# Performance work log

Hardware: AMD Instinct MI355X
Metric: run time of the kernel (lower is better)

Reference implementation:

```python
import jax, jax.numpy as jnp
import numpy as np

H = 4           # LSTM hidden size
T = 200         # seq len (T * H == 800, required by the reshape)
FEAT = 800      # flattened feature size into the linear
OUT = 28        # linear output dim


def run_lstm_layer(x, Wih, Whh, bih, bhh):
    """Single LSTM layer, PyTorch gate order (i, f, g, o). x: [B, T, I] -> [B, T, H]."""
    B = x.shape[0]
    xT = jnp.swapaxes(x, 0, 1)  # [T, B, I]
    h0 = jnp.zeros((B, H), x.dtype)
    c0 = jnp.zeros((B, H), x.dtype)
    b = bih + bhh  # [4H]

    def step(carry, xt):
        h, c = carry
        gates = xt @ Wih.T + h @ Whh.T + b  # [B, 4H]
        i, f, g, o = jnp.split(gates, 4, axis=-1)
        i = jax.nn.sigmoid(i)
        f = jax.nn.sigmoid(f)
        g = jnp.tanh(g)
        o = jax.nn.sigmoid(o)
        c = f * c + i * g
        h = o * jnp.tanh(c)
        return (h, c), h

    _, hs = jax.lax.scan(step, (h0, c0), xT)  # hs: [T, B, H]
    return jnp.swapaxes(hs, 0, 1)  # [B, T, H]


def setup_inputs() -> dict:
    key = jax.random.key(0)
    ks = jax.random.split(key, 12)
    B, I = 32768, 4
    s_lstm = 1.0 / np.sqrt(H)     # torch LSTM init bound
    s_lin = 1.0 / np.sqrt(FEAT)   # torch Linear init bound

    def u(k, shape, s):
        return jax.random.uniform(k, shape, jnp.float32, -s, s)

    return {
        "x": jax.random.normal(ks[0], (B, T, I), jnp.float32),
        "Wih0": u(ks[1], (4 * H, I), s_lstm),
        "Whh0": u(ks[2], (4 * H, H), s_lstm),
        "bih0": u(ks[3], (4 * H,), s_lstm),
        "bhh0": u(ks[4], (4 * H,), s_lstm),
        "Wih1": u(ks[5], (4 * H, H), s_lstm),
        "Whh1": u(ks[6], (4 * H, H), s_lstm),
        "bih1": u(ks[7], (4 * H,), s_lstm),
        "bhh1": u(ks[8], (4 * H,), s_lstm),
        "Wout": u(ks[9], (OUT, FEAT), s_lin),
        "bout": u(ks[10], (OUT,), s_lin),
    }


def reference(x, Wih0, Whh0, bih0, bhh0, Wih1, Whh1, bih1, bhh1, Wout, bout):
    h1 = run_lstm_layer(x, Wih0, Whh0, bih0, bhh0)   # [B, T, H]
    h2 = run_lstm_layer(h1, Wih1, Whh1, bih1, bhh1)  # [B, T, H]
    feat = h2.reshape(-1, FEAT)                      # [B, 800] since T*H == 800
    return feat @ Wout.T + bout                      # [B, 28]
```

## Files before the change

kernel.cpp:

```cpp
#include <hip/hip_runtime.h>

#define T_STEPS 200
#define OUTD 28

typedef float f2 __attribute__((ext_vector_type(2)));

template<int SRC>
__device__ __forceinline__ float qb(float v) {
    return __int_as_float(__builtin_amdgcn_update_dpp(
        0, __float_as_int(v), SRC * 0x55, 0xF, 0xF, true));
}

#define PIN2(v) asm volatile("" : "+v"(v))

__global__ void transpose_wout(const float* __restrict__ Wout, float* __restrict__ Wt) {
    int idx = blockIdx.x * 256 + threadIdx.x;
    if (idx < T_STEPS * OUTD * 4) {
        int t = idx / (OUTD * 4);
        int r = idx - t * (OUTD * 4);
        int j = r >> 2, c = r & 3;
        Wt[idx] = Wout[j * 800 + 4 * t + c];
    }
}

__device__ __forceinline__ void layer_step2(const f2 (&wia)[4], const f2 (&wib)[4],
                                            const f2 (&wha)[4], const f2 (&whb)[4],
                                            const f2 (&bb)[4],
                                            f2 ina0, f2 inb0, f2 ina1, f2 inb1,
                                            f2& ha0, f2& hb0, f2& ha1, f2& hb1,
                                            float& c0, float& c1)
{
    float g0[4], g1[4];
#pragma unroll
    for (int gi = 0; gi < 4; ++gi) {
        f2 s0 = bb[gi];
        f2 s1 = bb[gi];
        s0 += wia[gi] * ina0;  s1 += wia[gi] * ina1;
        s0 += wib[gi] * inb0;  s1 += wib[gi] * inb1;
        s0 += wha[gi] * ha0;   s1 += wha[gi] * ha1;
        s0 += whb[gi] * hb0;   s1 += whb[gi] * hb1;
        g0[gi] = s0.x + s0.y;  g1[gi] = s1.x + s1.y;
    }
    float Ei0 = __builtin_amdgcn_exp2f(g0[0]), Ei1 = __builtin_amdgcn_exp2f(g1[0]);
    float Ef0 = __builtin_amdgcn_exp2f(g0[1]), Ef1 = __builtin_amdgcn_exp2f(g1[1]);
    float Eg0 = __builtin_amdgcn_exp2f(g0[2]), Eg1 = __builtin_amdgcn_exp2f(g1[2]);
    float Eo0 = __builtin_amdgcn_exp2f(g0[3]), Eo1 = __builtin_amdgcn_exp2f(g1[3]);
    float Ai0 = 1.0f + Ei0,  Ai1 = 1.0f + Ei1;
    float Af0 = 1.0f + Ef0,  Af1 = 1.0f + Ef1;
    float Ag0 = 1.0f + Eg0,  Ag1 = 1.0f + Eg1;
    float Ao0 = 1.0f + Eo0,  Ao1 = 1.0f + Eo1;
    float P0 = Ai0 * Ag0,    P1 = Ai1 * Ag1;
    float n0 = c0 * P0 + (Eg0 - 1.0f) * Af0;
    float n1 = c1 * P1 + (Eg1 - 1.0f) * Af1;
    float r0 = __builtin_amdgcn_rcpf(P0 * Af0);
    float r1 = __builtin_amdgcn_rcpf(P1 * Af1);
    c0 = n0 * r0;
    c1 = n1 * r1;
    float cc0 = __builtin_amdgcn_fmed3f(c0, -16.0f, 16.0f);
    float cc1 = __builtin_amdgcn_fmed3f(c1, -16.0f, 16.0f);
    float Ec0 = __builtin_amdgcn_exp2f(2.8853900817779268f * cc0);
    float Ec1 = __builtin_amdgcn_exp2f(2.8853900817779268f * cc1);
    float q0 = __builtin_amdgcn_rcpf(Ao0 * (1.0f + Ec0));
    float q1 = __builtin_amdgcn_rcpf(Ao1 * (1.0f + Ec1));
    float ho0 = (Ec0 - 1.0f) * q0;
    float ho1 = (Ec1 - 1.0f) * q1;
    ha0 = f2{qb<0>(ho0), qb<1>(ho0)};
    ha1 = f2{qb<0>(ho1), qb<1>(ho1)};
    hb0 = f2{qb<2>(ho0), qb<3>(ho0)};
    hb1 = f2{qb<2>(ho1), qb<3>(ho1)};
}

template<bool PREF>
__device__ __forceinline__ void full_step(
    const f2 (&wi0a)[4], const f2 (&wi0b)[4], const f2 (&wh0a)[4], const f2 (&wh0b)[4],
    const f2 (&wi1a)[4], const f2 (&wi1b)[4], const f2 (&wh1a)[4], const f2 (&wh1b)[4],
    const f2 (&b0)[4], const f2 (&b1)[4],
    f2& h1a0, f2& h1b0, f2& h2a0, f2& h2b0, float& c10, float& c20,
    f2& h1a1, f2& h1b1, f2& h2a1, f2& h2b1, float& c11, float& c21,
    f2 (&acc0)[7], f2 (&acc1)[7],
    float4& xs0, float4& xs1,
    const char* xp, unsigned xo0, unsigned xo1, int tpf,
    const char* wtp, unsigned w_off)
{
    float4 wo[7];
#pragma unroll
    for (int jj = 0; jj < 7; ++jj)
        wo[jj] = *(const float4*)(wtp + w_off + jj * 16);

    f2 xa0 = f2{xs0.x, xs0.y}, xb0 = f2{xs0.z, xs0.w};
    f2 xa1 = f2{xs1.x, xs1.y}, xb1 = f2{xs1.z, xs1.w};

    layer_step2(wi0a, wi0b, wh0a, wh0b, b0,
                xa0, xb0, xa1, xb1,
                h1a0, h1b0, h1a1, h1b1, c10, c11);

    if (PREF) {
        xs0 = *(const float4*)(xp + xo0 + (size_t)tpf * 16);
        xs1 = *(const float4*)(xp + xo1 + (size_t)tpf * 16);
    }

    layer_step2(wi1a, wi1b, wh1a, wh1b, b1,
                h1a0, h1b0, h1a1, h1b1,
                h2a0, h2b0, h2a1, h2b1, c20, c21);

#pragma unroll
    for (int jj = 0; jj < 7; ++jj) {
        f2 wa = f2{wo[jj].x, wo[jj].y};
        f2 wb = f2{wo[jj].z, wo[jj].w};
        acc0[jj] += wa * h2a0; acc0[jj] += wb * h2b0;
        acc1[jj] += wa * h2a1; acc1[jj] += wb * h2b1;
    }
}

__global__ __launch_bounds__(256)
__attribute__((amdgpu_waves_per_eu(1, 1)))
void lstm2_fused(const float* __restrict__ x,
                 const float* __restrict__ Wih0, const float* __restrict__ Whh0,
                 const float* __restrict__ bih0, const float* __restrict__ bhh0,
                 const float* __restrict__ Wih1, const float* __restrict__ Whh1,
                 const float* __restrict__ bih1, const float* __restrict__ bhh1,
                 const float* __restrict__ Wt,   const float* __restrict__ bout,
                 float* __restrict__ out, int batch)
{
    const int tid = blockIdx.x * 256 + threadIdx.x;
    const int quad = tid >> 2;
    const int k = tid & 3;
    const int e0 = quad * 2, e1 = e0 + 1;
    if (e1 >= batch) return;

    f2 wi0a[4], wi0b[4], wh0a[4], wh0b[4];
    f2 wi1a[4], wi1b[4], wh1a[4], wh1b[4];
    f2 b0[4], b1[4];
#pragma unroll
    for (int gi = 0; gi < 4; ++gi) {
        const int row = gi * 4 + k;
        const float sc = (gi == 2) ? 2.8853900817779268f : -1.4426950408889634f;
        float4 a = ((const float4*)Wih0)[row];
        float4 c = ((const float4*)Whh0)[row];
        float4 d = ((const float4*)Wih1)[row];
        float4 e = ((const float4*)Whh1)[row];
        wi0a[gi] = f2{a.x * sc, a.y * sc}; wi0b[gi] = f2{a.z * sc, a.w * sc};
        wh0a[gi] = f2{c.x * sc, c.y * sc}; wh0b[gi] = f2{c.z * sc, c.w * sc};
        wi1a[gi] = f2{d.x * sc, d.y * sc}; wi1b[gi] = f2{d.z * sc, d.w * sc};
        wh1a[gi] = f2{e.x * sc, e.y * sc}; wh1b[gi] = f2{e.z * sc, e.w * sc};
        b0[gi] = f2{(bih0[row] + bhh0[row]) * sc, 0.0f};
        b1[gi] = f2{(bih1[row] + bhh1[row]) * sc, 0.0f};
    }
#pragma unroll
    for (int gi = 0; gi < 4; ++gi) {
        PIN2(wi0a[gi]); PIN2(wi0b[gi]); PIN2(wh0a[gi]); PIN2(wh0b[gi]);
        PIN2(wi1a[gi]); PIN2(wi1b[gi]); PIN2(wh1a[gi]); PIN2(wh1b[gi]);
        PIN2(b0[gi]);   PIN2(b1[gi]);
    }

    f2 acc0[7], acc1[7];
#pragma unroll
    for (int jj = 0; jj < 7; ++jj) {
        float bj = bout[k * 7 + jj];
        acc0[jj] = f2{bj, 0.0f};
        acc1[jj] = f2{bj, 0.0f};
    }

    f2 h1a0 = f2{0,0}, h1b0 = f2{0,0}, h2a0 = f2{0,0}, h2b0 = f2{0,0};
    f2 h1a1 = f2{0,0}, h1b1 = f2{0,0}, h2a1 = f2{0,0}, h2b1 = f2{0,0};
    float c10 = 0.0f, c20 = 0.0f, c11 = 0.0f, c21 = 0.0f;

    const char* xp  = (const char*)x;
    const unsigned xo0 = (unsigned)e0 * 3200u;
    const unsigned xo1 = (unsigned)e1 * 3200u;
    const char* wtp = (const char*)Wt;
    const unsigned w_off = (unsigned)k * 112u;

    float4 xv0 = *(const float4*)(xp + xo0);
    float4 xv1 = *(const float4*)(xp + xo1);
    float4 xn0 = *(const float4*)(xp + xo0 + 16);
    float4 xn1 = *(const float4*)(xp + xo1 + 16);

    for (int t = 0; t < T_STEPS - 2; t += 2) {
        full_step<true>(wi0a, wi0b, wh0a, wh0b, wi1a, wi1b, wh1a, wh1b, b0, b1,
                        h1a0, h1b0, h2a0, h2b0, c10, c20,
                        h1a1, h1b1, h2a1, h2b1, c11, c21,
                        acc0, acc1, xv0, xv1, xp, xo0, xo1, t + 2, wtp, w_off);
        wtp += OUTD * 16;
        full_step<true>(wi0a, wi0b, wh0a, wh0b, wi1a, wi1b, wh1a, wh1b, b0, b1,
                        h1a0, h1b0, h2a0, h2b0, c10, c20,
                        h1a1, h1b1, h2a1, h2b1, c11, c21,
                        acc0, acc1, xn0, xn1, xp, xo0, xo1, t + 3, wtp, w_off);
        wtp += OUTD * 16;
    }
    full_step<false>(wi0a, wi0b, wh0a, wh0b, wi1a, wi1b, wh1a, wh1b, b0, b1,
                     h1a0, h1b0, h2a0, h2b0, c10, c20,
                     h1a1, h1b1, h2a1, h2b1, c11, c21,
                     acc0, acc1, xv0, xv1, xp, xo0, xo1, 0, wtp, w_off);
    wtp += OUTD * 16;
    full_step<false>(wi0a, wi0b, wh0a, wh0b, wi1a, wi1b, wh1a, wh1b, b0, b1,
                     h1a0, h1b0, h2a0, h2b0, c10, c20,
                     h1a1, h1b1, h2a1, h2b1, c11, c21,
                     acc0, acc1, xn0, xn1, xp, xo0, xo1, 0, wtp, w_off);

    float* op0 = out + (size_t)e0 * OUTD + k * 7;
    float* op1 = out + (size_t)e1 * OUTD + k * 7;
#pragma unroll
    for (int jj = 0; jj < 7; ++jj) {
        op0[jj] = acc0[jj].x + acc0[jj].y;
        op1[jj] = acc1[jj].x + acc1[jj].y;
    }
}

extern "C" void kernel_launch(void* const* d_in, const int* in_sizes, int n_in,
                              void* d_out, int out_size, void* d_ws, size_t ws_size,
                              hipStream_t stream) {
    const float* x    = (const float*)d_in[0];
    const float* Wih0 = (const float*)d_in[1];
    const float* Whh0 = (const float*)d_in[2];
    const float* bih0 = (const float*)d_in[3];
    const float* bhh0 = (const float*)d_in[4];
    const float* Wih1 = (const float*)d_in[5];
    const float* Whh1 = (const float*)d_in[6];
    const float* bih1 = (const float*)d_in[7];
    const float* bhh1 = (const float*)d_in[8];
    const float* Wout = (const float*)d_in[9];
    const float* bout = (const float*)d_in[10];
    float* out = (float*)d_out;
    float* Wt  = (float*)d_ws;

    transpose_wout<<<(T_STEPS * OUTD * 4 + 255) / 256, 256, 0, stream>>>(Wout, Wt);

    const int batch = in_sizes[0] / (T_STEPS * 4);
    const int threads = (batch / 2) * 4;
    const int grid = threads / 256;
    lstm2_fused<<<grid, 256, 0, stream>>>(
        x, Wih0, Whh0, bih0, bhh0, Wih1, Whh1, bih1, bhh1, Wt, bout, out, batch);
}
```

Baseline: 234.9 us.

## Split LSTM layers across producer/consumer waves with LDS double-buffered pipeline

Each block now has 512 threads. Four waves compute layer 1 and four waves compute layer 2 one timestep behind, exchanging hidden states through double-buffered shared memory with a barrier per step. The output linear accumulation is split between the two wave groups, which lowers per-thread register pressure and gives more concurrent waves. The cost is a __syncthreads per timestep and extra LDS traffic, and batch must be divisible by 128.

```diff
diff --git a/kernel.cpp b/kernel.cpp
--- a/kernel.cpp
+++ b/kernel.cpp
@@ -23,12 +23,13 @@
     }
 }
 
-__device__ __forceinline__ void layer_step2(const f2 (&wia)[4], const f2 (&wib)[4],
-                                            const f2 (&wha)[4], const f2 (&whb)[4],
-                                            const f2 (&bb)[4],
-                                            f2 ina0, f2 inb0, f2 ina1, f2 inb1,
-                                            f2& ha0, f2& hb0, f2& ha1, f2& hb1,
-                                            float& c0, float& c1)
+__device__ __forceinline__ void layer_pair(const f2 (&wia)[4], const f2 (&wib)[4],
+                                           const f2 (&wha)[4], const f2 (&whb)[4],
+                                           const f2 (&bb)[4],
+                                           f2 ina0, f2 inb0, f2 ina1, f2 inb1,
+                                           f2& ha0, f2& hb0, f2& ha1, f2& hb1,
+                                           float& c0, float& c1,
+                                           float& o0, float& o1)
 {
     float g0[4], g1[4];
 #pragma unroll
@@ -56,64 +57,29 @@
     float r1 = __builtin_amdgcn_rcpf(P1 * Af1);
     c0 = n0 * r0;
     c1 = n1 * r1;
-    float cc0 = __builtin_amdgcn_fmed3f(c0, -16.0f, 16.0f);
-    float cc1 = __builtin_amdgcn_fmed3f(c1, -16.0f, 16.0f);
-    float Ec0 = __builtin_amdgcn_exp2f(2.8853900817779268f * cc0);
-    float Ec1 = __builtin_amdgcn_exp2f(2.8853900817779268f * cc1);
+    float cl0 = __builtin_amdgcn_fmed3f(c0, -16.0f, 16.0f);
+    float cl1 = __builtin_amdgcn_fmed3f(c1, -16.0f, 16.0f);
+    float Ec0 = __builtin_amdgcn_exp2f(2.8853900817779268f * cl0);
+    float Ec1 = __builtin_amdgcn_exp2f(2.8853900817779268f * cl1);
     float q0 = __builtin_amdgcn_rcpf(Ao0 * (1.0f + Ec0));
     float q1 = __builtin_amdgcn_rcpf(Ao1 * (1.0f + Ec1));
     float ho0 = (Ec0 - 1.0f) * q0;
     float ho1 = (Ec1 - 1.0f) * q1;
+    o0 = ho0;
+    o1 = ho1;
     ha0 = f2{qb<0>(ho0), qb<1>(ho0)};
+    hb0 = f2{qb<2>(ho0), qb<3>(ho0)};
     ha1 = f2{qb<0>(ho1), qb<1>(ho1)};
-    hb0 = f2{qb<2>(ho0), qb<3>(ho0)};
     hb1 = f2{qb<2>(ho1), qb<3>(ho1)};
 }
 
-template<bool PREF>
-__device__ __forceinline__ void full_step(
-    const f2 (&wi0a)[4], const f2 (&wi0b)[4], const f2 (&wh0a)[4], const f2 (&wh0b)[4],
-    const f2 (&wi1a)[4], const f2 (&wi1b)[4], const f2 (&wh1a)[4], const f2 (&wh1b)[4],
-    const f2 (&b0)[4], const f2 (&b1)[4],
-    f2& h1a0, f2& h1b0, f2& h2a0, f2& h2b0, float& c10, float& c20,
-    f2& h1a1, f2& h1b1, f2& h2a1, f2& h2b1, float& c11, float& c21,
-    f2 (&acc0)[7], f2 (&acc1)[7],
-    float4& xs0, float4& xs1,
-    const char* xp, unsigned xo0, unsigned xo1, int tpf,
-    const char* wtp, unsigned w_off)
-{
-    float4 wo[7];
-#pragma unroll
-    for (int jj = 0; jj < 7; ++jj)
-        wo[jj] = *(const float4*)(wtp + w_off + jj * 16);
-
-    f2 xa0 = f2{xs0.x, xs0.y}, xb0 = f2{xs0.z, xs0.w};
-    f2 xa1 = f2{xs1.x, xs1.y}, xb1 = f2{xs1.z, xs1.w};
-
-    layer_step2(wi0a, wi0b, wh0a, wh0b, b0,
-                xa0, xb0, xa1, xb1,
-                h1a0, h1b0, h1a1, h1b1, c10, c11);
-
-    if (PREF) {
-        xs0 = *(const float4*)(xp + xo0 + (size_t)tpf * 16);
-        xs1 = *(const float4*)(xp + xo1 + (size_t)tpf * 16);
-    }
-
-    layer_step2(wi1a, wi1b, wh1a, wh1b, b1,
-                h1a0, h1b0, h1a1, h1b1,
-                h2a0, h2b0, h2a1, h2b1, c20, c21);
-
-#pragma unroll
-    for (int jj = 0; jj < 7; ++jj) {
-        f2 wa = f2{wo[jj].x, wo[jj].y};
-        f2 wb = f2{wo[jj].z, wo[jj].w};
-        acc0[jj] += wa * h2a0; acc0[jj] += wb * h2b0;
-        acc1[jj] += wa * h2a1; acc1[jj] += wb * h2b1;
-    }
-}
-
-__global__ __launch_bounds__(256)
-__attribute__((amdgpu_waves_per_eu(1, 1)))
+__device__ __forceinline__ void lin_acc(f2& a, const float4& wo, f2 ha, f2 hb) {
+    a += f2{wo.x, wo.y} * ha;
+    a += f2{wo.z, wo.w} * hb;
+}
+
+__global__ __launch_bounds__(512)
+__attribute__((amdgpu_waves_per_eu(2, 2)))
 void lstm2_fused(const float* __restrict__ x,
                  const float* __restrict__ Wih0, const float* __restrict__ Whh0,
                  const float* __restrict__ bih0, const float* __restrict__ bhh0,
@@ -122,88 +88,180 @@
                  const float* __restrict__ Wt,   const float* __restrict__ bout,
                  float* __restrict__ out, int batch)
 {
-    const int tid = blockIdx.x * 256 + threadIdx.x;
-    const int quad = tid >> 2;
-    const int k = tid & 3;
-    const int e0 = quad * 2, e1 = e0 + 1;
-    if (e1 >= batch) return;
-
-    f2 wi0a[4], wi0b[4], wh0a[4], wh0b[4];
-    f2 wi1a[4], wi1b[4], wh1a[4], wh1b[4];
-    f2 b0[4], b1[4];
+    __shared__ __align__(16) float h1buf[2][128][4];
+    __shared__ __align__(16) float h2buf[2][128][4];
+
+    const int tidx = threadIdx.x;
+    const int wid  = tidx >> 6;
+    const int k    = tidx & 3;
+    const int q    = (tidx >> 2) & 15;
+    const int le0  = (wid & 3) * 32 + q * 2;
+    const int le1  = le0 + 1;
+    const int e0   = blockIdx.x * 128 + le0;
+    const int e1   = e0 + 1;
+    const bool isP = (wid < 4);
+
+    const float4* Wi = isP ? (const float4*)Wih0 : (const float4*)Wih1;
+    const float4* Wh = isP ? (const float4*)Whh0 : (const float4*)Whh1;
+    const float*  bi = isP ? bih0 : bih1;
+    const float*  bh = isP ? bhh0 : bhh1;
+
+    f2 wia[4], wib[4], wha[4], whb[4], bb[4];
 #pragma unroll
     for (int gi = 0; gi < 4; ++gi) {
         const int row = gi * 4 + k;
         const float sc = (gi == 2) ? 2.8853900817779268f : -1.4426950408889634f;
-        float4 a = ((const float4*)Wih0)[row];
-        float4 c = ((const float4*)Whh0)[row];
-        float4 d = ((const float4*)Wih1)[row];
-        float4 e = ((const float4*)Whh1)[row];
-        wi0a[gi] = f2{a.x * sc, a.y * sc}; wi0b[gi] = f2{a.z * sc, a.w * sc};
-        wh0a[gi] = f2{c.x * sc, c.y * sc}; wh0b[gi] = f2{c.z * sc, c.w * sc};
-        wi1a[gi] = f2{d.x * sc, d.y * sc}; wi1b[gi] = f2{d.z * sc, d.w * sc};
-        wh1a[gi] = f2{e.x * sc, e.y * sc}; wh1b[gi] = f2{e.z * sc, e.w * sc};
-        b0[gi] = f2{(bih0[row] + bhh0[row]) * sc, 0.0f};
-        b1[gi] = f2{(bih1[row] + bhh1[row]) * sc, 0.0f};
-    }
-#pragma unroll
-    for (int gi = 0; gi < 4; ++gi) {
-        PIN2(wi0a[gi]); PIN2(wi0b[gi]); PIN2(wh0a[gi]); PIN2(wh0b[gi]);
-        PIN2(wi1a[gi]); PIN2(wi1b[gi]); PIN2(wh1a[gi]); PIN2(wh1b[gi]);
-        PIN2(b0[gi]);   PIN2(b1[gi]);
-    }
-
-    f2 acc0[7], acc1[7];
-#pragma unroll
-    for (int jj = 0; jj < 7; ++jj) {
-        float bj = bout[k * 7 + jj];
-        acc0[jj] = f2{bj, 0.0f};
-        acc1[jj] = f2{bj, 0.0f};
-    }
-
-    f2 h1a0 = f2{0,0}, h1b0 = f2{0,0}, h2a0 = f2{0,0}, h2b0 = f2{0,0};
-    f2 h1a1 = f2{0,0}, h1b1 = f2{0,0}, h2a1 = f2{0,0}, h2b1 = f2{0,0};
-    float c10 = 0.0f, c20 = 0.0f, c11 = 0.0f, c21 = 0.0f;
+        float4 a = Wi[row];
+        float4 c = Wh[row];
+        wia[gi] = f2{a.x * sc, a.y * sc}; wib[gi] = f2{a.z * sc, a.w * sc};
+        wha[gi] = f2{c.x * sc, c.y * sc}; whb[gi] = f2{c.z * sc, c.w * sc};
+        bb[gi]  = f2{(bi[row] + bh[row]) * sc, 0.0f};
+        PIN2(wia[gi]); PIN2(wib[gi]); PIN2(wha[gi]); PIN2(whb[gi]); PIN2(bb[gi]);
+    }
+
+    f2 acc[4][2];
+#pragma unroll
+    for (int jj = 0; jj < 4; ++jj) {
+        float bj = isP ? bout[k * 7 + jj]
+                       : (jj < 3 ? bout[k * 7 + 4 + jj] : 0.0f);
+        acc[jj][0] = f2{bj, 0.0f};
+        acc[jj][1] = f2{bj, 0.0f};
+    }
+
+    f2 ha0{0,0}, hb0{0,0}, ha1{0,0}, hb1{0,0};
+    float cs0 = 0.0f, cs1 = 0.0f;
+    float o0 = 0.0f, o1 = 0.0f;
 
     const char* xp  = (const char*)x;
+    const char* wtp = (const char*)Wt;
     const unsigned xo0 = (unsigned)e0 * 3200u;
     const unsigned xo1 = (unsigned)e1 * 3200u;
-    const char* wtp = (const char*)Wt;
-    const unsigned w_off = (unsigned)k * 112u;
-
-    float4 xv0 = *(const float4*)(xp + xo0);
-    float4 xv1 = *(const float4*)(xp + xo1);
-    float4 xn0 = *(const float4*)(xp + xo0 + 16);
-    float4 xn1 = *(const float4*)(xp + xo1 + 16);
-
-    for (int t = 0; t < T_STEPS - 2; t += 2) {
-        full_step<true>(wi0a, wi0b, wh0a, wh0b, wi1a, wi1b, wh1a, wh1b, b0, b1,
-                        h1a0, h1b0, h2a0, h2b0, c10, c20,
-                        h1a1, h1b1, h2a1, h2b1, c11, c21,
-                        acc0, acc1, xv0, xv1, xp, xo0, xo1, t + 2, wtp, w_off);
-        wtp += OUTD * 16;
-        full_step<true>(wi0a, wi0b, wh0a, wh0b, wi1a, wi1b, wh1a, wh1b, b0, b1,
-                        h1a0, h1b0, h2a0, h2b0, c10, c20,
-                        h1a1, h1b1, h2a1, h2b1, c11, c21,
-                        acc0, acc1, xn0, xn1, xp, xo0, xo1, t + 3, wtp, w_off);
-        wtp += OUTD * 16;
-    }
-    full_step<false>(wi0a, wi0b, wh0a, wh0b, wi1a, wi1b, wh1a, wh1b, b0, b1,
-                     h1a0, h1b0, h2a0, h2b0, c10, c20,
-                     h1a1, h1b1, h2a1, h2b1, c11, c21,
-                     acc0, acc1, xv0, xv1, xp, xo0, xo1, 0, wtp, w_off);
-    wtp += OUTD * 16;
-    full_step<false>(wi0a, wi0b, wh0a, wh0b, wi1a, wi1b, wh1a, wh1b, b0, b1,
-                     h1a0, h1b0, h2a0, h2b0, c10, c20,
-                     h1a1, h1b1, h2a1, h2b1, c11, c21,
-                     acc0, acc1, xn0, xn1, xp, xo0, xo1, 0, wtp, w_off);
-
-    float* op0 = out + (size_t)e0 * OUTD + k * 7;
-    float* op1 = out + (size_t)e1 * OUTD + k * 7;
-#pragma unroll
-    for (int jj = 0; jj < 7; ++jj) {
-        op0[jj] = acc0[jj].x + acc0[jj].y;
-        op1[jj] = acc1[jj].x + acc1[jj].y;
+    const unsigned wA  = (unsigned)k * 112u;
+    const unsigned wB  = (unsigned)k * 112u + 64u;
+
+    float4 xv0, xv1, xn0, xn1;
+    if (isP) {
+        xv0 = *(const float4*)(xp + xo0);
+        xv1 = *(const float4*)(xp + xo1);
+        xn0 = *(const float4*)(xp + xo0 + 16);
+        xn1 = *(const float4*)(xp + xo1 + 16);
+    }
+
+#define P_PHASE(PE, XS0, XS1, TPF, DOL1, DOLIN, DOPREF)                        \
+    do {                                                                       \
+        float4 H20, H21, wq0, wq1, wq2, wq3;                                   \
+        if (DOLIN) {                                                           \
+            H20 = *(const float4*)&h2buf[PE][le0][0];                          \
+            H21 = *(const float4*)&h2buf[PE][le1][0];                          \
+            wq0 = *(const float4*)(wtp + wA);                                  \
+            wq1 = *(const float4*)(wtp + wA + 16);                             \
+            wq2 = *(const float4*)(wtp + wA + 32);                             \
+            wq3 = *(const float4*)(wtp + wA + 48);                             \
+        }                                                                      \
+        if (DOL1) {                                                            \
+            layer_pair(wia, wib, wha, whb, bb,                                 \
+                       f2{XS0.x, XS0.y}, f2{XS0.z, XS0.w},                     \
+                       f2{XS1.x, XS1.y}, f2{XS1.z, XS1.w},                     \
+                       ha0, hb0, ha1, hb1, cs0, cs1, o0, o1);                  \
+            h1buf[PE][le0][k] = o0;                                            \
+            h1buf[PE][le1][k] = o1;                                            \
+            if (DOPREF) {                                                      \
+                XS0 = *(const float4*)(xp + xo0 + (size_t)(TPF) * 16);         \
+                XS1 = *(const float4*)(xp + xo1 + (size_t)(TPF) * 16);         \
+            }                                                                  \
+        }                                                                      \
+        if (DOLIN) {                                                           \
+            f2 Ga0{H20.x, H20.y}, Gb0{H20.z, H20.w};                           \
+            f2 Ga1{H21.x, H21.y}, Gb1{H21.z, H21.w};                           \
+            lin_acc(acc[0][0], wq0, Ga0, Gb0);                                 \
+            lin_acc(acc[1][0], wq1, Ga0, Gb0);                                 \
+            lin_acc(acc[2][0], wq2, Ga0, Gb0);                                 \
+            lin_acc(acc[3][0], wq3, Ga0, Gb0);                                 \
+            lin_acc(acc[0][1], wq0, Ga1, Gb1);                                 \
+            lin_acc(acc[1][1], wq1, Ga1, Gb1);                                 \
+            lin_acc(acc[2][1], wq2, Ga1, Gb1);                                 \
+            lin_acc(acc[3][1], wq3, Ga1, Gb1);                                 \
+        }                                                                      \
+    } while (0)
+
+#define C_PHASE(PE, DOL2, DOLIN)                                               \
+    do {                                                                       \
+        float4 H10, H11;                                                       \
+        if (DOL2) {                                                            \
+            H10 = *(const float4*)&h1buf[(PE) ^ 1][le0][0];                    \
+            H11 = *(const float4*)&h1buf[(PE) ^ 1][le1][0];                    \
+        }                                                                      \
+        if (DOLIN) {                                                           \
+               \
+            float4 wq0 = *(const float4*)(wtp + wB);                           \
+            float4 wq1 = *(const float4*)(wtp + wB + 16);                      \
+            float4 wq2 = *(const float4*)(wtp + wB + 32);                      \
+            lin_acc(acc[0][0], wq0, ha0, hb0);                                 \
+            lin_acc(acc[1][0], wq1, ha0, hb0);                                 \
+            lin_acc(acc[2][0], wq2, ha0, hb0);                                 \
+            lin_acc(acc[0][1], wq0, ha1, hb1);                                 \
+            lin_acc(acc[1][1], wq1, ha1, hb1);                                 \
+            lin_acc(acc[2][1], wq2, ha1, hb1);                                 \
+        }                                                                      \
+        if (DOL2) {                                                            \
+            layer_pair(wia, wib, wha, whb, bb,                                 \
+                       f2{H10.x, H10.y}, f2{H10.z, H10.w},                     \
+                       f2{H11.x, H11.y}, f2{H11.z, H11.w},                     \
+                       ha0, hb0, ha1, hb1, cs0, cs1, o0, o1);                  \
+            h2buf[(PE) ^ 1][le0][k] = o0;                                      \
+            h2buf[(PE) ^ 1][le1][k] = o1;                                      \
+        }                                                                      \
+    } while (0)
+
+    if (isP) P_PHASE(0, xv0, xv1, 2, true, false, true);
+    __syncthreads();
+    if (isP) P_PHASE(1, xn0, xn1, 3, true, false, true);
+    else     C_PHASE(1, true, false);
+    __syncthreads();
+    for (int t = 2; t <= 196; t += 2) {
+        if (isP) P_PHASE(0, xv0, xv1, t + 2, true, true, true);
+        else     C_PHASE(0, true, true);
+        wtp += 448;
+        __syncthreads();
+        if (isP) P_PHASE(1, xn0, xn1, t + 3, true, true, true);
+        else     C_PHASE(1, true, true);
+        wtp += 448;
+        __syncthreads();
+    }
+    if (isP) P_PHASE(0, xv0, xv1, 0, true, true, false);
+    else     C_PHASE(0, true, true);
+    wtp += 448;
+    __syncthreads();
+    if (isP) P_PHASE(1, xn0, xn1, 0, true, true, false);
+    else     C_PHASE(1, true, true);
+    wtp += 448;
+    __syncthreads();
+    if (isP) P_PHASE(0, xv0, xv1, 0, false, true, false);
+    else     C_PHASE(0, true, true);
+    wtp += 448;
+    __syncthreads();
+    if (isP) P_PHASE(1, xn0, xn1, 0, false, true, false);
+    else     C_PHASE(1, false, true);
+
+#undef P_PHASE
+#undef C_PHASE
+
+    if (isP) {
+        float* op0 = out + (size_t)e0 * OUTD + k * 7;
+        float* op1 = out + (size_t)e1 * OUTD + k * 7;
+#pragma unroll
+        for (int jj = 0; jj < 4; ++jj) {
+            op0[jj] = acc[jj][0].x + acc[jj][0].y;
+            op1[jj] = acc[jj][1].x + acc[jj][1].y;
+        }
+    } else {
+        float* op0 = out + (size_t)e0 * OUTD + k * 7 + 4;
+        float* op1 = out + (size_t)e1 * OUTD + k * 7 + 4;
+#pragma unroll
+        for (int jj = 0; jj < 3; ++jj) {
+            op0[jj] = acc[jj][0].x + acc[jj][0].y;
+            op1[jj] = acc[jj][1].x + acc[jj][1].y;
+        }
     }
 }
 
@@ -227,8 +285,7 @@
     transpose_wout<<<(T_STEPS * OUTD * 4 + 255) / 256, 256, 0, stream>>>(Wout, Wt);
 
     const int batch = in_sizes[0] / (T_STEPS * 4);
-    const int threads = (batch / 2) * 4;
-    const int grid = threads / 256;
-    lstm2_fused<<<grid, 256, 0, stream>>>(
+    const int grid = batch / 128;
+    lstm2_fused<<<grid, 512, 0, stream>>>(
         x, Wih0, Whh0, bih0, bhh0, Wih1, Whh1, bih1, bhh1, Wt, bout, out, batch);
 }
```

After: 258.7 us. 1.1x slower.
